# Optimization experiments

Hardware: AMD Instinct MI355X
Metric: run time of the kernel (lower is better)

Reference implementation:

```python
import jax, jax.numpy as jnp
import numpy as np

N_VERTICES = 2000
N_SENSORY = 784
N_EDGES = 500_000
BATCH = 32
T_STEPS = 5
LR_VALUES = 0.1


def setup_inputs() -> dict:
    key = jax.random.key(0)
    k1, k2, k3 = jax.random.split(key, 3)
    values = jax.random.normal(k1, (BATCH, N_VERTICES), dtype=jnp.float32)
    # weight_init 'normal 0.0' -> std = max(0.01, 0) = 0.01 in the torch module
    weights = jax.random.normal(k2, (N_EDGES,), dtype=jnp.float32) * 0.01
    edge_index = jax.random.randint(k3, (2, N_EDGES), 0, N_VERTICES, dtype=jnp.int32)
    # sensory nodes (first 784) are clamped; only internal nodes update
    update_mask = jnp.arange(N_VERTICES) >= N_SENSORY  # bool [N]
    return {
        "values": values,
        "weights": weights,
        "edge_index": edge_index,
        "update_mask": update_mask,
        "T": T_STEPS,
    }


def reference(values, weights, edge_index, update_mask, T):
    """Iterative predictive-coding message passing.

    Each step:
      pred_i  = sum_{e: dst(e)=i} w_e * f(values[src(e)])   (gather-mul-scatter)
      err     = values - pred
      back_j  = sum_{e: src(e)=j} w_e * err[dst(e)]          (reverse scatter)
      dv      = err - f'(values) * back                      (dE/dx)
      values  = values - lr * dv   (sensory nodes clamped)
    """
    src, dst = edge_index[0], edge_index[1]
    n = values.shape[1]
    mask = update_mask[None, :]

    def step(v, _):
        fx = jnp.tanh(v)                                   # [B, N]
        msg = weights[None, :] * fx[:, src]                # [B, E]
        pred = jax.ops.segment_sum(msg.T, dst, num_segments=n).T  # [B, N]
        err = v - pred                                     # [B, N]
        w_err = weights[None, :] * err[:, dst]             # [B, E]
        back = jax.ops.segment_sum(w_err.T, src, num_segments=n).T  # [B, N]
        fprime = 1.0 - fx * fx                             # tanh'
        dv = err - fprime * back
        v_new = jnp.where(mask, v - LR_VALUES * dv, v)
        return v_new, None

    v_final, _ = jax.lax.scan(step, values, None, length=T)
    return v_final
```

## Files before the change

kernel.cpp:

```cpp
#include <hip/hip_runtime.h>
#include <hip/hip_bf16.h>


#define N_V     2000
#define N_SENS  784
#define N_INT   (N_V - N_SENS)
#define N_E     500000
#define T_STEPS 5
#define LR_VAL  0.1f
#define NVB     (N_V * 32)
#define NVH     (N_V * 16)
#define KP      2016
#define NCH     63
#define NT1     125
#define NT2     76
#define FRAG_N  (2 * NCH * 64 * 8)
#define NBLK    250
#define EPB     2000

typedef float  f32x4 __attribute__((ext_vector_type(4)));
typedef short  s16x8 __attribute__((ext_vector_type(8)));

__device__ __forceinline__ float bits_to_f32(unsigned u) {
    union { unsigned u; float f; } c; c.u = u; return c.f;
}
__device__ __forceinline__ unsigned f32_to_bits(float f) {
    union { float f; unsigned u; } c; c.f = f; return c.u;
}
__device__ __forceinline__ unsigned short f32_to_bf16(float f) {
    unsigned u = f32_to_bits(f);
    return (unsigned short)((u + 0x7FFFu + ((u >> 16) & 1u)) >> 16);
}
__device__ __forceinline__ float bf16_to_f32(unsigned short s) {
    return bits_to_f32((unsigned)s << 16);
}

__device__ __forceinline__ int aposKB(int k, int b) {
    int c = k >> 5, q = (k >> 3) & 3, j = k & 7;
    int h = b >> 4, m = b & 15;
    return (((h * NCH + c) * 64) + q * 16 + m) * 8 + j;
}


__global__ __launch_bounds__(256) void k_cnt(const int* __restrict__ dst,
                                             int* __restrict__ cnt_g,
                                             unsigned short* __restrict__ fxA,
                                             unsigned short* __restrict__ errA) {
    __shared__ int cnt[NT1];
    int b = blockIdx.x;
    {
        int t = b * 256 + threadIdx.x;
        if (t < 16 * 32) {
            int k = 2000 + (t >> 5), bb = t & 31;
            fxA[aposKB(k, bb)] = 0;
            errA[aposKB(k, bb)] = 0;
        }
    }
    for (int i = threadIdx.x; i < NT1; i += 256) cnt[i] = 0;
    __syncthreads();
    int base = b * EPB;
    for (int e = base + threadIdx.x; e < base + EPB; e += 256)
        atomicAdd(&cnt[dst[e] >> 4], 1);
    __syncthreads();
    for (int t = threadIdx.x; t < NT1; t += 256)
        cnt_g[t * 256 + b] = cnt[t];
}

__global__ __launch_bounds__(256) void k_scan_a(const int* __restrict__ cnt_g,
                                                int* __restrict__ base_g,
                                                int* __restrict__ totals) {
    __shared__ int sh[256];
    int t = blockIdx.x, tid = threadIdx.x;
    int v = (tid < NBLK) ? cnt_g[t * 256 + tid] : 0;
    sh[tid] = v;
    __syncthreads();
    for (int off = 1; off < 256; off <<= 1) {
        int x = (tid >= off) ? sh[tid - off] : 0;
        __syncthreads();
        sh[tid] += x;
        __syncthreads();
    }
    if (tid < NBLK) base_g[t * 256 + tid] = sh[tid] - v;
    if (tid == 255) totals[t] = sh[255];
}

__global__ void k_scan_b(const int* __restrict__ totals, int* __restrict__ tile_start) {
    if (threadIdx.x == 0 && blockIdx.x == 0) {
        int acc = 0;
        for (int t = 0; t < NT1; ++t) { tile_start[t] = acc; acc += totals[t]; }
        tile_start[NT1] = acc;
    }
}

__global__ __launch_bounds__(256) void k_place(
        const int* __restrict__ src, const int* __restrict__ dst,
        const float* __restrict__ w, const int* __restrict__ base_g,
        const int* __restrict__ tile_start, unsigned* __restrict__ pk_g) {
    __shared__ int cur[NT1];
    int b = blockIdx.x;
    for (int t = threadIdx.x; t < NT1; t += 256)
        cur[t] = tile_start[t] + base_g[t * 256 + b];
    __syncthreads();
    int base = b * EPB;
    for (int e = base + threadIdx.x; e < base + EPB; e += 256) {
        int d = dst[e];
        unsigned pk = ((unsigned)f32_to_bf16(w[e]) << 16)
                    | ((unsigned)(d & 15) << 11) | (unsigned)src[e];
        int p = atomicAdd(&cur[d >> 4], 1);
        pk_g[p] = pk;
    }
}

__global__ __launch_bounds__(256) void k_build(
        const unsigned* __restrict__ pk_g, const int* __restrict__ tile_start,
        uint4* __restrict__ WAbf4, unsigned short* __restrict__ WAd) {
    __shared__ float acc[8][KP];
    int tile = blockIdx.x >> 1, half = blockIdx.x & 1;
    for (int i = threadIdx.x; i < 8 * KP / 4; i += 256)
        ((float4*)&acc[0][0])[i] = make_float4(0.f, 0.f, 0.f, 0.f);
    __syncthreads();
    int beg = tile_start[tile], end = tile_start[tile + 1];
    for (int e = beg + threadIdx.x; e < end; e += 256) {
        unsigned pk = pk_g[e];
        int row = (int)((pk >> 11) & 15u);
        if ((row >> 3) == half)
            atomicAdd(&acc[row & 7][pk & 0x7FFu], bf16_to_f32((unsigned short)(pk >> 16)));
    }
    __syncthreads();
    for (int i = threadIdx.x; i < 8 * 252; i += 256) {
        int rr = i / 252, g = i - rr * 252;
        int c = g >> 2, q = g & 3;
        int col = g * 8;
        unsigned short r[8];
        #pragma unroll
        for (int j = 0; j < 8; ++j) r[j] = f32_to_bf16(acc[rr][col + j]);
        uint4 val = *(const uint4*)r;
        int m = half * 8 + rr;
        WAbf4[((tile * NCH + c) * 64) + q * 16 + m] = val;
        *(uint4*)(WAd + (size_t)(tile * 16 + m) * KP + col) = val;
    }
}

__global__ void k_trB(const unsigned short* __restrict__ WAd, uint4* __restrict__ WBf4) {
    int t = blockIdx.x * blockDim.x + threadIdx.x;
    if (t < NT2 * NCH * 64) {
        int tile = t / (NCH * 64);
        int rem = t - tile * (NCH * 64);
        int c = rem >> 6, l = rem & 63;
        int jcol = N_SENS + tile * 16 + (l & 15);
        int k0 = c * 32 + (l >> 4) * 8;
        unsigned short r[8];
        #pragma unroll
        for (int j = 0; j < 8; ++j)
            r[j] = (k0 + j < N_V) ? WAd[(size_t)(k0 + j) * KP + jcol] : (unsigned short)0;
        WBf4[t] = *(const uint4*)r;
    }
}

__global__ void k_init(const float* __restrict__ vin, float* __restrict__ v,
                       unsigned short* __restrict__ fxA, float* __restrict__ out) {
    int t = blockIdx.x * blockDim.x + threadIdx.x;
    if (t < NVB) {
        float x = vin[t];
        int b = t / N_V;
        int i = t - b * N_V;
        v[(i << 5) + b] = x;
        fxA[aposKB(i, b)] = f32_to_bf16(tanhf(x));
        if (i < N_SENS) out[t] = x;
    }
}

__global__ __launch_bounds__(256) void k_gemm1(
        const uint4* __restrict__ WAbf4, const uint4* __restrict__ fxA4,
        const float* __restrict__ v_cur, unsigned short* __restrict__ errA) {
    __shared__ float red[1300];
    int bx = blockIdx.x, tid = threadIdx.x;
    int w = tid >> 6, l = tid & 63;
    int tile = bx >> 1, h = bx & 1;
    int cbeg = w * 16;
    const uint4* bp = WAbf4 + (size_t)tile * NCH * 64 + cbeg * 64 + l;
    const uint4* ap = fxA4 + (size_t)h * NCH * 64 + cbeg * 64 + l;
    f32x4 acc = {0.f, 0.f, 0.f, 0.f};
    #pragma unroll
    for (int cc = 0; cc < 16; ++cc) {
        if (cbeg + cc < NCH) {
            uint4 bfrag = bp[cc * 64];
            uint4 a = ap[cc * 64];
            acc = __builtin_amdgcn_mfma_f32_16x16x32_bf16(
                      *(s16x8*)&a, *(s16x8*)&bfrag, acc, 0, 0, 0);
        }
    }
    float* my = &red[w * 325 + l * 5];
    #pragma unroll
    for (int r = 0; r < 4; ++r) my[r] = acc[r];
    __syncthreads();
    if (w == 0) {
        float s[4];
        #pragma unroll
        for (int r = 0; r < 4; ++r)
            s[r] = red[l * 5 + r] + red[325 + l * 5 + r]
                 + red[650 + l * 5 + r] + red[975 + l * 5 + r];
        int i = tile * 16 + (l & 15);
        int q = l >> 4;
        int c2 = i >> 5, q2 = (i >> 3) & 3, j2 = i & 7;
        const float4 v4 = *(const float4*)(v_cur + (i << 5) + h * 16 + q * 4);
        int base = ((h * NCH + c2) * 64 + q2 * 16) * 8 + j2;
        errA[base + (q * 4 + 0) * 8] = f32_to_bf16(v4.x - s[0]);
        errA[base + (q * 4 + 1) * 8] = f32_to_bf16(v4.y - s[1]);
        errA[base + (q * 4 + 2) * 8] = f32_to_bf16(v4.z - s[2]);
        errA[base + (q * 4 + 3) * 8] = f32_to_bf16(v4.w - s[3]);
    }
}

__global__ __launch_bounds__(256) void k_gemm2(
        const uint4* __restrict__ WBf4, const uint4* __restrict__ errA4,
        unsigned short* __restrict__ errA, unsigned short* __restrict__ fxA,
        float* __restrict__ v_cur, float* __restrict__ out, int final_step) {
    __shared__ float red[1300];
    int bx = blockIdx.x, tid = threadIdx.x;
    int w = tid >> 6, l = tid & 63;
    int tile = bx >> 1, h = bx & 1;
    int cbeg = w * 16;
    const uint4* bp = WBf4 + (size_t)tile * NCH * 64 + cbeg * 64 + l;
    const uint4* ap = errA4 + (size_t)h * NCH * 64 + cbeg * 64 + l;
    f32x4 acc = {0.f, 0.f, 0.f, 0.f};
    #pragma unroll
    for (int cc = 0; cc < 16; ++cc) {
        if (cbeg + cc < NCH) {
            uint4 bfrag = bp[cc * 64];
            uint4 a = ap[cc * 64];
            acc = __builtin_amdgcn_mfma_f32_16x16x32_bf16(
                      *(s16x8*)&a, *(s16x8*)&bfrag, acc, 0, 0, 0);
        }
    }
    float* my = &red[w * 325 + l * 5];
    #pragma unroll
    for (int r = 0; r < 4; ++r) my[r] = acc[r];
    __syncthreads();
    if (w == 0) {
        float s[4];
        #pragma unroll
        for (int r = 0; r < 4; ++r)
            s[r] = red[l * 5 + r] + red[325 + l * 5 + r]
                 + red[650 + l * 5 + r] + red[975 + l * 5 + r];
        int j = N_SENS + tile * 16 + (l & 15);
        int q = l >> 4;
        int c2 = j >> 5, q2 = (j >> 3) & 3, j2 = j & 7;
        float4 v4 = *(const float4*)(v_cur + (j << 5) + h * 16 + q * 4);
        int base = ((h * NCH + c2) * 64 + q2 * 16) * 8 + j2;
        float vv[4] = {v4.x, v4.y, v4.z, v4.w};
        #pragma unroll
        for (int r = 0; r < 4; ++r) {
            float e0 = bf16_to_f32(errA[base + (q * 4 + r) * 8]);
            float fxv = tanhf(vv[r]);
            float vn = vv[r] - LR_VAL * (e0 - (1.f - fxv * fxv) * s[r]);
            vv[r] = vn;
            fxA[base + (q * 4 + r) * 8] = f32_to_bf16(tanhf(vn));
        }
        float4 o = {vv[0], vv[1], vv[2], vv[3]};
        *(float4*)(v_cur + (j << 5) + h * 16 + q * 4) = o;
        if (final_step) {
            #pragma unroll
            for (int r = 0; r < 4; ++r) {
                int b = h * 16 + q * 4 + r;
                out[b * N_V + j] = vv[r];
            }
        }
    }
}


__global__ void k_zero_i32(int* a, int n) {
    int t = blockIdx.x * blockDim.x + threadIdx.x;
    if (t < n) a[t] = 0;
}

__global__ void k_hist(const int* __restrict__ src, const int* __restrict__ dst,
                       int* cnt_dst, int* cnt_src) {
    int e = blockIdx.x * blockDim.x + threadIdx.x;
    if (e < N_E) {
        atomicAdd(&cnt_dst[dst[e]], 1);
        atomicAdd(&cnt_src[src[e]], 1);
    }
}

__global__ __launch_bounds__(1024) void k_scan(int* cnt_a, int* rp_a,
                                               int* cnt_b, int* rp_b) {
    __shared__ int sh[1024];
    int t = threadIdx.x;
    for (int pass = 0; pass < 2; ++pass) {
        int* cnt = pass ? cnt_b : cnt_a;
        int* rp  = pass ? rp_b  : rp_a;
        int i0 = 2 * t, i1 = 2 * t + 1;
        int c0 = (i0 < N_V) ? cnt[i0] : 0;
        int c1 = (i1 < N_V) ? cnt[i1] : 0;
        __syncthreads();
        sh[t] = c0 + c1;
        __syncthreads();
        for (int off = 1; off < 1024; off <<= 1) {
            int v = (t >= off) ? sh[t - off] : 0;
            __syncthreads();
            sh[t] += v;
            __syncthreads();
        }
        int incl = sh[t];
        int e0 = incl - (c0 + c1);
        int e1 = e0 + c0;
        if (i0 <= N_V) rp[i0] = e0;
        if (i1 <= N_V) rp[i1] = e1;
        if (i0 < N_V) cnt[i0] = e0;
        if (i1 < N_V) cnt[i1] = e1;
    }
}

__global__ void k_scatter(const int* __restrict__ src, const int* __restrict__ dst,
                          const float* __restrict__ w,
                          int* cur_dst, int* cur_src,
                          unsigned* __restrict__ pk_dst, unsigned* __restrict__ pk_src) {
    int e = blockIdx.x * blockDim.x + threadIdx.x;
    if (e < N_E) {
        int s = src[e], d = dst[e];
        unsigned wbits = (unsigned)f32_to_bf16(w[e]);
        int p = atomicAdd(&cur_dst[d], 1);
        pk_dst[p] = (wbits << 16) | (unsigned)s;
        int q = atomicAdd(&cur_src[s], 1);
        pk_src[q] = (wbits << 16) | (unsigned)d;
    }
}

__global__ void k_cast_in(const float* __restrict__ vin, float* __restrict__ v) {
    int t = blockIdx.x * blockDim.x + threadIdx.x;
    if (t < NVB) {
        int i = t >> 5, b = t & 31;
        v[t] = vin[b * N_V + i];
    }
}

__global__ void k_fx_csr(const float* __restrict__ v, unsigned short* __restrict__ fx) {
    int t = blockIdx.x * blockDim.x + threadIdx.x;
    if (t < NVB) {
        int i = t >> 5, b = t & 31;
        int h = b >> 4, b16 = b & 15;
        fx[h * NVH + i * 16 + b16] = f32_to_bf16(tanhf(v[t]));
    }
}

__global__ __launch_bounds__(256) void k_pred_err(
        const float* __restrict__ v, const unsigned short* __restrict__ fx,
        const int* __restrict__ rp, const unsigned* __restrict__ pk,
        unsigned short* __restrict__ err) {
    __shared__ unsigned short tab[NVH];
    int h  = blockIdx.x / 250;
    int vg = blockIdx.x % 250;
    {
        const uint4* g = (const uint4*)(fx + h * NVH);
        uint4* l = (uint4*)tab;
        for (int i = threadIdx.x; i < NVH / 8; i += 256) l[i] = g[i];
    }
    __syncthreads();
    int wave = threadIdx.x >> 6;
    int lane = threadIdx.x & 63;
    int b16 = lane & 15, epar = lane >> 4;
    for (int k = 0; k < 2; ++k) {
        int vid = vg * 8 + wave * 2 + k;
        int beg = rp[vid], end = rp[vid + 1];
        float sum = 0.f;
        for (int e = beg + epar; e < end; e += 4) {
            unsigned p = pk[e];
            float w = bits_to_f32(p & 0xFFFF0000u);
            int nb = (int)(p & 0xFFFFu);
            sum += w * bf16_to_f32(tab[nb * 16 + b16]);
        }
        sum += __shfl_xor(sum, 16, 64);
        sum += __shfl_xor(sum, 32, 64);
        if (epar == 0) {
            float vo = v[(vid << 5) + h * 16 + b16];
            err[h * NVH + vid * 16 + b16] = f32_to_bf16(vo - sum);
        }
    }
}

__global__ __launch_bounds__(256) void k_back_upd(
        const unsigned short* __restrict__ fx, const unsigned short* __restrict__ err,
        const int* __restrict__ rp, const unsigned* __restrict__ pk,
        float* __restrict__ v) {
    __shared__ unsigned short tab[NVH];
    int h  = blockIdx.x / 152;
    int vg = blockIdx.x % 152;
    {
        const uint4* g = (const uint4*)(err + h * NVH);
        uint4* l = (uint4*)tab;
        for (int i = threadIdx.x; i < NVH / 8; i += 256) l[i] = g[i];
    }
    __syncthreads();
    int wave = threadIdx.x >> 6;
    int lane = threadIdx.x & 63;
    int b16 = lane & 15, epar = lane >> 4;
    for (int k = 0; k < 2; ++k) {
        int vid = N_SENS + vg * 8 + wave * 2 + k;
        if (vid >= N_V) continue;
        int beg = rp[vid], end = rp[vid + 1];
        float sum = 0.f;
        for (int e = beg + epar; e < end; e += 4) {
            unsigned p = pk[e];
            float w = bits_to_f32(p & 0xFFFF0000u);
            int nb = (int)(p & 0xFFFFu);
            sum += w * bf16_to_f32(tab[nb * 16 + b16]);
        }
        sum += __shfl_xor(sum, 16, 64);
        sum += __shfl_xor(sum, 32, 64);
        if (epar == 0) {
            float e0  = bf16_to_f32(tab[vid * 16 + b16]);
            float fxv = bf16_to_f32(fx[h * NVH + vid * 16 + b16]);
            float dv = e0 - (1.f - fxv * fxv) * sum;
            v[(vid << 5) + h * 16 + b16] -= LR_VAL * dv;
        }
    }
}

__global__ void k_out_fb(const float* __restrict__ v, float* __restrict__ out) {
    int t = blockIdx.x * blockDim.x + threadIdx.x;
    if (t < NVB) {
        int b = t / N_V;
        int i = t - b * N_V;
        out[t] = v[(i << 5) + b];
    }
}


extern "C" void kernel_launch(void* const* d_in, const int* in_sizes, int n_in,
                              void* d_out, int out_size, void* d_ws, size_t ws_size,
                              hipStream_t stream) {
    const float* vals = (const float*)d_in[0];
    const float* wts  = (const float*)d_in[1];
    const int* ei = (const int*)d_in[2];
    const int* src = ei;
    const int* dst = ei + N_E;
    float* out = (float*)d_out;

    const int EB = (N_E + 255) / 256;

    const size_t WABF_T = (size_t)NT1 * NCH * 64;
    const size_t WBF_T  = (size_t)NT2 * NCH * 64;
    const size_t WAD_N  = (size_t)N_V * KP;
    const size_t need = (size_t)N_E * 4 + 2 * NT1 * 256 * 4 + 512 * 4
                      + WAD_N * 2 + WABF_T * 16 + WBF_T * 16
                      + 2 * (size_t)FRAG_N * 2 + NVB * 4 + 256;

    if (ws_size >= need) {
        unsigned* pk_g = (unsigned*)d_ws;
        int* cnt_g  = (int*)(pk_g + N_E);
        int* base_g = cnt_g + NT1 * 256;
        int* totals = base_g + NT1 * 256;
        int* tile_start = totals + 128;
        unsigned short* WAd = (unsigned short*)(tile_start + 384);
        uint4* WAbf4 = (uint4*)(WAd + WAD_N);
        uint4* WBf4  = WAbf4 + WABF_T;
        unsigned short* fxA  = (unsigned short*)(WBf4 + WBF_T);
        unsigned short* errA = fxA + FRAG_N;
        float* v_cur = (float*)(errA + FRAG_N);

        k_cnt<<<NBLK, 256, 0, stream>>>(dst, cnt_g, fxA, errA);
        k_scan_a<<<NT1, 256, 0, stream>>>(cnt_g, base_g, totals);
        k_scan_b<<<1, 64, 0, stream>>>(totals, tile_start);
        k_place<<<NBLK, 256, 0, stream>>>(src, dst, wts, base_g, tile_start, pk_g);
        k_build<<<2 * NT1, 256, 0, stream>>>(pk_g, tile_start, WAbf4, WAd);
        k_trB<<<(int)((WBF_T + 255) / 256), 256, 0, stream>>>(WAd, WBf4);
        k_init<<<250, 256, 0, stream>>>(vals, v_cur, fxA, out);

        for (int t = 0; t < T_STEPS; ++t) {
            k_gemm1<<<250, 256, 0, stream>>>(WAbf4, (const uint4*)fxA, v_cur, errA);
            k_gemm2<<<152, 256, 0, stream>>>(WBf4, (const uint4*)errA, errA, fxA,
                                             v_cur, out, (t == T_STEPS - 1) ? 1 : 0);
        }
    } else {
        float* v_cur = (float*)d_ws;
        unsigned short* fx_g  = (unsigned short*)(v_cur + NVB);
        unsigned short* err_g = fx_g + NVB;
        int* rp_dst  = (int*)(err_g + NVB);
        int* rp_src  = rp_dst + 2048;
        int* cur_dst = rp_src + 2048;
        int* cur_src = cur_dst + 2048;
        unsigned* pk_dst = (unsigned*)(cur_src + 2048);
        unsigned* pk_src = pk_dst + N_E;

        k_zero_i32<<<16, 256, 0, stream>>>(cur_dst, 4096);
        k_hist<<<EB, 256, 0, stream>>>(src, dst, cur_dst, cur_src);
        k_scan<<<1, 1024, 0, stream>>>(cur_dst, rp_dst, cur_src, rp_src);
        k_scatter<<<EB, 256, 0, stream>>>(src, dst, wts, cur_dst, cur_src,
                                          pk_dst, pk_src);
        k_cast_in<<<250, 256, 0, stream>>>(vals, v_cur);
        for (int t = 0; t < T_STEPS; ++t) {
            k_fx_csr<<<250, 256, 0, stream>>>(v_cur, fx_g);
            k_pred_err<<<500, 256, 0, stream>>>(v_cur, fx_g, rp_dst, pk_dst, err_g);
            k_back_upd<<<304, 256, 0, stream>>>(fx_g, err_g, rp_src, pk_src, v_cur);
        }
        k_out_fb<<<250, 256, 0, stream>>>(v_cur, out);
    }
}
```

Before: 172.4 us.

## Fuse timestep loop into persistent kernel with grid barriers and LDS-resident weights

Replaces the ten per-step GEMM launches with one persistent kernel of 201 blocks. The first 125 blocks hold a forward weight tile in LDS and the rest hold a backward tile, and the steps are separated by atomic-counter grid barriers. This removes repeated launch overhead and repeated global weight reads. In exchange, half the blocks idle during each phase, and the design assumes all blocks can be resident at once, otherwise the spin barrier deadlocks.

```diff
diff --git a/kernel.cpp b/kernel.cpp
--- a/kernel.cpp
+++ b/kernel.cpp
@@ -17,6 +17,7 @@
 #define FRAG_N  (2 * NCH * 64 * 8)
 #define NBLK    250
 #define EPB     2000
+#define NBLK_P  (NT1 + NT2)
 
 typedef float  f32x4 __attribute__((ext_vector_type(4)));
 typedef short  s16x8 __attribute__((ext_vector_type(8)));
@@ -89,6 +90,7 @@
         int acc = 0;
         for (int t = 0; t < NT1; ++t) { tile_start[t] = acc; acc += totals[t]; }
         tile_start[NT1] = acc;
+        tile_start[256] = 0;
     }
 }
 
@@ -170,102 +172,120 @@
     }
 }
 
-__global__ __launch_bounds__(256) void k_gemm1(
-        const uint4* __restrict__ WAbf4, const uint4* __restrict__ fxA4,
-        const float* __restrict__ v_cur, unsigned short* __restrict__ errA) {
-    __shared__ float red[1300];
-    int bx = blockIdx.x, tid = threadIdx.x;
-    int w = tid >> 6, l = tid & 63;
-    int tile = bx >> 1, h = bx & 1;
-    int cbeg = w * 16;
-    const uint4* bp = WAbf4 + (size_t)tile * NCH * 64 + cbeg * 64 + l;
-    const uint4* ap = fxA4 + (size_t)h * NCH * 64 + cbeg * 64 + l;
-    f32x4 acc = {0.f, 0.f, 0.f, 0.f};
-    #pragma unroll
-    for (int cc = 0; cc < 16; ++cc) {
-        if (cbeg + cc < NCH) {
-            uint4 bfrag = bp[cc * 64];
-            uint4 a = ap[cc * 64];
-            acc = __builtin_amdgcn_mfma_f32_16x16x32_bf16(
-                      *(s16x8*)&a, *(s16x8*)&bfrag, acc, 0, 0, 0);
-        }
-    }
-    float* my = &red[w * 325 + l * 5];
-    #pragma unroll
-    for (int r = 0; r < 4; ++r) my[r] = acc[r];
-    __syncthreads();
-    if (w == 0) {
-        float s[4];
-        #pragma unroll
-        for (int r = 0; r < 4; ++r)
-            s[r] = red[l * 5 + r] + red[325 + l * 5 + r]
-                 + red[650 + l * 5 + r] + red[975 + l * 5 + r];
-        int i = tile * 16 + (l & 15);
-        int q = l >> 4;
-        int c2 = i >> 5, q2 = (i >> 3) & 3, j2 = i & 7;
-        const float4 v4 = *(const float4*)(v_cur + (i << 5) + h * 16 + q * 4);
-        int base = ((h * NCH + c2) * 64 + q2 * 16) * 8 + j2;
-        errA[base + (q * 4 + 0) * 8] = f32_to_bf16(v4.x - s[0]);
-        errA[base + (q * 4 + 1) * 8] = f32_to_bf16(v4.y - s[1]);
-        errA[base + (q * 4 + 2) * 8] = f32_to_bf16(v4.z - s[2]);
-        errA[base + (q * 4 + 3) * 8] = f32_to_bf16(v4.w - s[3]);
-    }
-}
-
-__global__ __launch_bounds__(256) void k_gemm2(
-        const uint4* __restrict__ WBf4, const uint4* __restrict__ errA4,
-        unsigned short* __restrict__ errA, unsigned short* __restrict__ fxA,
-        float* __restrict__ v_cur, float* __restrict__ out, int final_step) {
-    __shared__ float red[1300];
-    int bx = blockIdx.x, tid = threadIdx.x;
-    int w = tid >> 6, l = tid & 63;
-    int tile = bx >> 1, h = bx & 1;
-    int cbeg = w * 16;
-    const uint4* bp = WBf4 + (size_t)tile * NCH * 64 + cbeg * 64 + l;
-    const uint4* ap = errA4 + (size_t)h * NCH * 64 + cbeg * 64 + l;
-    f32x4 acc = {0.f, 0.f, 0.f, 0.f};
-    #pragma unroll
-    for (int cc = 0; cc < 16; ++cc) {
-        if (cbeg + cc < NCH) {
-            uint4 bfrag = bp[cc * 64];
-            uint4 a = ap[cc * 64];
-            acc = __builtin_amdgcn_mfma_f32_16x16x32_bf16(
-                      *(s16x8*)&a, *(s16x8*)&bfrag, acc, 0, 0, 0);
-        }
-    }
-    float* my = &red[w * 325 + l * 5];
-    #pragma unroll
-    for (int r = 0; r < 4; ++r) my[r] = acc[r];
-    __syncthreads();
-    if (w == 0) {
-        float s[4];
-        #pragma unroll
-        for (int r = 0; r < 4; ++r)
-            s[r] = red[l * 5 + r] + red[325 + l * 5 + r]
-                 + red[650 + l * 5 + r] + red[975 + l * 5 + r];
-        int j = N_SENS + tile * 16 + (l & 15);
-        int q = l >> 4;
-        int c2 = j >> 5, q2 = (j >> 3) & 3, j2 = j & 7;
-        float4 v4 = *(const float4*)(v_cur + (j << 5) + h * 16 + q * 4);
-        int base = ((h * NCH + c2) * 64 + q2 * 16) * 8 + j2;
-        float vv[4] = {v4.x, v4.y, v4.z, v4.w};
-        #pragma unroll
-        for (int r = 0; r < 4; ++r) {
-            float e0 = bf16_to_f32(errA[base + (q * 4 + r) * 8]);
-            float fxv = tanhf(vv[r]);
-            float vn = vv[r] - LR_VAL * (e0 - (1.f - fxv * fxv) * s[r]);
-            vv[r] = vn;
-            fxA[base + (q * 4 + r) * 8] = f32_to_bf16(tanhf(vn));
-        }
-        float4 o = {vv[0], vv[1], vv[2], vv[3]};
-        *(float4*)(v_cur + (j << 5) + h * 16 + q * 4) = o;
-        if (final_step) {
+__device__ __forceinline__ void gbar(int* cnt, int target) {
+    __syncthreads();
+    if (threadIdx.x == 0) {
+        __hip_atomic_fetch_add(cnt, 1, __ATOMIC_RELEASE, __HIP_MEMORY_SCOPE_AGENT);
+        while (__hip_atomic_load(cnt, __ATOMIC_RELAXED, __HIP_MEMORY_SCOPE_AGENT) < target)
+            __builtin_amdgcn_s_sleep(2);
+        __builtin_amdgcn_fence(__ATOMIC_ACQUIRE, "agent");
+    }
+    __syncthreads();
+}
+
+__global__ __launch_bounds__(512, 1) void k_loop(
+        const uint4* __restrict__ WAbf4, const uint4* __restrict__ WBf4,
+        unsigned short* fxA, unsigned short* errA,
+        float* v_cur, float* __restrict__ out, int* cnt) {
+    __shared__ uint4 Wlds[NCH * 64];
+    __shared__ float red[2600];
+    const int bx = blockIdx.x;
+    const int tid = threadIdx.x;
+    const bool is_dst = (bx < NT1);
+    const int tile = is_dst ? bx : bx - NT1;
+    {
+        const uint4* Wg = (is_dst ? WAbf4 : WBf4) + (size_t)tile * (NCH * 64);
+        for (int i = tid; i < NCH * 64; i += 512) Wlds[i] = Wg[i];
+    }
+    const int w = tid >> 6, l = tid & 63;
+    const int h = w >> 2, w4 = w & 3;
+    const int cbeg = w4 * 16;
+    float* my = &red[h * 1300 + w4 * 325 + l * 5];
+    int bar = 0;
+    __syncthreads();
+
+    for (int t = 0; t < T_STEPS; ++t) {
+        if (is_dst) {
+            const uint4* ap = (const uint4*)fxA + (size_t)h * (NCH * 64) + cbeg * 64 + l;
+            f32x4 acc = {0.f, 0.f, 0.f, 0.f};
             #pragma unroll
-            for (int r = 0; r < 4; ++r) {
-                int b = h * 16 + q * 4 + r;
-                out[b * N_V + j] = vv[r];
+            for (int cc = 0; cc < 16; ++cc) {
+                if (cbeg + cc < NCH) {
+                    uint4 bfrag = Wlds[(cbeg + cc) * 64 + l];
+                    uint4 a = ap[cc * 64];
+                    acc = __builtin_amdgcn_mfma_f32_16x16x32_bf16(
+                              *(s16x8*)&a, *(s16x8*)&bfrag, acc, 0, 0, 0);
+                }
             }
-        }
+            #pragma unroll
+            for (int r = 0; r < 4; ++r) my[r] = acc[r];
+            __syncthreads();
+            if (w4 == 0) {
+                float s[4];
+                #pragma unroll
+                for (int r = 0; r < 4; ++r)
+                    s[r] = red[h * 1300 + l * 5 + r] + red[h * 1300 + 325 + l * 5 + r]
+                         + red[h * 1300 + 650 + l * 5 + r] + red[h * 1300 + 975 + l * 5 + r];
+                int i = tile * 16 + (l & 15);
+                int q = l >> 4;
+                int c2 = i >> 5, q2 = (i >> 3) & 3, j2 = i & 7;
+                const float4 v4 = *(const float4*)(v_cur + (i << 5) + h * 16 + q * 4);
+                int base = ((h * NCH + c2) * 64 + q2 * 16) * 8 + j2;
+                errA[base + (q * 4 + 0) * 8] = f32_to_bf16(v4.x - s[0]);
+                errA[base + (q * 4 + 1) * 8] = f32_to_bf16(v4.y - s[1]);
+                errA[base + (q * 4 + 2) * 8] = f32_to_bf16(v4.z - s[2]);
+                errA[base + (q * 4 + 3) * 8] = f32_to_bf16(v4.w - s[3]);
+            }
+        }
+        ++bar; gbar(cnt, bar * NBLK_P);
+
+        if (!is_dst) {
+            const uint4* ap = (const uint4*)errA + (size_t)h * (NCH * 64) + cbeg * 64 + l;
+            f32x4 acc = {0.f, 0.f, 0.f, 0.f};
+            #pragma unroll
+            for (int cc = 0; cc < 16; ++cc) {
+                if (cbeg + cc < NCH) {
+                    uint4 bfrag = Wlds[(cbeg + cc) * 64 + l];
+                    uint4 a = ap[cc * 64];
+                    acc = __builtin_amdgcn_mfma_f32_16x16x32_bf16(
+                              *(s16x8*)&a, *(s16x8*)&bfrag, acc, 0, 0, 0);
+                }
+            }
+            #pragma unroll
+            for (int r = 0; r < 4; ++r) my[r] = acc[r];
+            __syncthreads();
+            if (w4 == 0) {
+                float s[4];
+                #pragma unroll
+                for (int r = 0; r < 4; ++r)
+                    s[r] = red[h * 1300 + l * 5 + r] + red[h * 1300 + 325 + l * 5 + r]
+                         + red[h * 1300 + 650 + l * 5 + r] + red[h * 1300 + 975 + l * 5 + r];
+                int j = N_SENS + tile * 16 + (l & 15);
+                int q = l >> 4;
+                int c2 = j >> 5, q2 = (j >> 3) & 3, j2 = j & 7;
+                float4 v4 = *(const float4*)(v_cur + (j << 5) + h * 16 + q * 4);
+                int base = ((h * NCH + c2) * 64 + q2 * 16) * 8 + j2;
+                float vv[4] = {v4.x, v4.y, v4.z, v4.w};
+                #pragma unroll
+                for (int r = 0; r < 4; ++r) {
+                    float e0 = bf16_to_f32(errA[base + (q * 4 + r) * 8]);
+                    float fxv = tanhf(vv[r]);
+                    float vn = vv[r] - LR_VAL * (e0 - (1.f - fxv * fxv) * s[r]);
+                    vv[r] = vn;
+                    fxA[base + (q * 4 + r) * 8] = f32_to_bf16(tanhf(vn));
+                }
+                float4 o = {vv[0], vv[1], vv[2], vv[3]};
+                *(float4*)(v_cur + (j << 5) + h * 16 + q * 4) = o;
+                if (t == T_STEPS - 1) {
+                    #pragma unroll
+                    for (int r = 0; r < 4; ++r) {
+                        int b = h * 16 + q * 4 + r;
+                        out[b * N_V + j] = vv[r];
+                    }
+                }
+            }
+        }
+        if (t < T_STEPS - 1) { ++bar; gbar(cnt, bar * NBLK_P); }
     }
 }
 
@@ -459,6 +479,7 @@
         unsigned short* fxA  = (unsigned short*)(WBf4 + WBF_T);
         unsigned short* errA = fxA + FRAG_N;
         float* v_cur = (float*)(errA + FRAG_N);
+        int* bar_cnt = tile_start + 256;
 
         k_cnt<<<NBLK, 256, 0, stream>>>(dst, cnt_g, fxA, errA);
         k_scan_a<<<NT1, 256, 0, stream>>>(cnt_g, base_g, totals);
@@ -468,11 +489,8 @@
         k_trB<<<(int)((WBF_T + 255) / 256), 256, 0, stream>>>(WAd, WBf4);
         k_init<<<250, 256, 0, stream>>>(vals, v_cur, fxA, out);
 
-        for (int t = 0; t < T_STEPS; ++t) {
-            k_gemm1<<<250, 256, 0, stream>>>(WAbf4, (const uint4*)fxA, v_cur, errA);
-            k_gemm2<<<152, 256, 0, stream>>>(WBf4, (const uint4*)errA, errA, fxA,
-                                             v_cur, out, (t == T_STEPS - 1) ? 1 : 0);
-        }
+        k_loop<<<NBLK_P, 512, 0, stream>>>(WAbf4, WBf4, fxA, errA, v_cur, out,
+                                           bar_cnt);
     } else {
         float* v_cur = (float*)d_ws;
         unsigned short* fx_g  = (unsigned short*)(v_cur + NVB);
```

Result: slower. 221.5 us (+28.5%).
